# Performance work log

Hardware: AMD Instinct MI355X
Metric: run time of the kernel (lower is better)

Reference implementation:

```python
import jax, jax.numpy as jnp
import numpy as np

N = 50000      # nodes
E = 500000     # edges (avg degree 10)
G = 64         # graphs (events)
IN = 7
H = 64
EPS = 1e-5


def setup_inputs() -> dict:
    key = jax.random.key(0)
    ks = iter(jax.random.split(key, 64))
    d = {}
    d["x"] = jax.random.normal(next(ks), (N, IN), jnp.float32)
    d["edge_index"] = jax.random.randint(next(ks), (2, E), 0, N, dtype=jnp.int32)
    d["batch"] = jnp.sort(jax.random.randint(next(ks), (N,), 0, G, dtype=jnp.int32))
    dims = [(IN, H), (H, 2 * H), (2 * H, 4 * H)]
    for i, (ic, oc) in enumerate(dims, 1):
        d[f"b{i}_W1"] = jax.random.normal(next(ks), (2 * ic, oc), jnp.float32) * 0.05
        d[f"b{i}_b1"] = jnp.zeros((oc,), jnp.float32)
        d[f"b{i}_g1"] = jnp.ones((oc,), jnp.float32)
        d[f"b{i}_beta1"] = jnp.zeros((oc,), jnp.float32)
        d[f"b{i}_W2"] = jax.random.normal(next(ks), (oc, oc), jnp.float32) * 0.05
        d[f"b{i}_b2"] = jnp.zeros((oc,), jnp.float32)
        d[f"b{i}_g2"] = jnp.ones((oc,), jnp.float32)
        d[f"b{i}_beta2"] = jnp.zeros((oc,), jnp.float32)
    d["head_W1"] = jax.random.normal(next(ks), (4 * H, 2 * H), jnp.float32) * 0.05
    d["head_b1"] = jnp.zeros((2 * H,), jnp.float32)
    d["head_W2"] = jax.random.normal(next(ks), (2 * H, 2), jnp.float32) * 0.05
    d["head_b2"] = jnp.zeros((2,), jnp.float32)
    return d


def _bn(h, g, b):
    # BatchNorm1d in training mode: batch statistics over edge dim
    m = h.mean(axis=0)
    v = h.var(axis=0)
    return (h - m) * jax.lax.rsqrt(v + EPS) * g + b


def _edgeconv(x, src, dst, W1, b1, g1, be1, W2, b2, g2, be2):
    # PyG EdgeConv: message = MLP(cat[x_i, x_j - x_i]), aggregated at target i=dst
    xi = x[dst]                                   # [E, C]
    xj = x[src]                                   # [E, C]
    e = jnp.concatenate([xi, xj - xi], axis=-1)   # [E, 2C]
    h = jax.nn.relu(_bn(e @ W1 + b1, g1, be1))
    h = jax.nn.relu(_bn(h @ W2 + b2, g2, be2))
    s = jax.ops.segment_sum(h, dst, num_segments=N)
    cnt = jax.ops.segment_sum(jnp.ones((h.shape[0],), h.dtype), dst, num_segments=N)
    return s / jnp.maximum(cnt, 1.0)[:, None]     # mean aggregation


def reference(x, edge_index, batch,
              b1_W1, b1_b1, b1_g1, b1_beta1, b1_W2, b1_b2, b1_g2, b1_beta2,
              b2_W1, b2_b1, b2_g1, b2_beta1, b2_W2, b2_b2, b2_g2, b2_beta2,
              b3_W1, b3_b1, b3_g1, b3_beta1, b3_W2, b3_b2, b3_g2, b3_beta2,
              head_W1, head_b1, head_W2, head_b2):
    src, dst = edge_index[0], edge_index[1]
    h = _edgeconv(x, src, dst, b1_W1, b1_b1, b1_g1, b1_beta1, b1_W2, b1_b2, b1_g2, b1_beta2)
    h = _edgeconv(h, src, dst, b2_W1, b2_b1, b2_g1, b2_beta1, b2_W2, b2_b2, b2_g2, b2_beta2)
    h = _edgeconv(h, src, dst, b3_W1, b3_b1, b3_g1, b3_beta1, b3_W2, b3_b2, b3_g2, b3_beta2)
    # global mean pool per graph
    s = jax.ops.segment_sum(h, batch, num_segments=G)
    cnt = jax.ops.segment_sum(jnp.ones((N,), h.dtype), batch, num_segments=G)
    g = s / jnp.maximum(cnt, 1.0)[:, None]        # [G, 256]
    # head (dropout is identity in eval)
    z = jax.nn.relu(g @ head_W1 + head_b1)
    return z @ head_W2 + head_b2                  # [G, 2]
```

## Files before the change

kernel.cpp:

```cpp
#include <hip/hip_runtime.h>
#include <stdint.h>

constexpr int NN = 50000;
constexpr int NE = 500000;
constexpr int NG = 64;
constexpr float BN_EPS = 1e-5f;
constexpr int ET = 32;

typedef __attribute__((ext_vector_type(8))) short bf16x8;
typedef __attribute__((ext_vector_type(4))) float f32x4;

__device__ inline float bf2f(unsigned short u) {
    return __uint_as_float(((unsigned int)u) << 16);
}
__device__ inline unsigned short f2bf_rne(float f) {
    unsigned int u = __float_as_uint(f);
    unsigned int r = (u + 0x7fffu + ((u >> 16) & 1u)) >> 16;
    return (unsigned short)r;
}

template<int CPT> __device__ inline void load_row(const float* p, float* o) {
    if constexpr (CPT == 2) { float2 v = *(const float2*)p; o[0]=v.x; o[1]=v.y; }
    else if constexpr (CPT == 4) { float4 v = *(const float4*)p; o[0]=v.x; o[1]=v.y; o[2]=v.z; o[3]=v.w; }
    else { load_row<4>(p, o); load_row<4>(p+4, o+4); }
}
template<int CPT> __device__ inline void store_row(float* p, const float* v) {
    if constexpr (CPT == 2) { *(float2*)p = make_float2(v[0], v[1]); }
    else if constexpr (CPT == 4) { *(float4*)p = make_float4(v[0], v[1], v[2], v[3]); }
    else { store_row<4>(p, v); store_row<4>(p+4, v+4); }
}

__global__ void k_zero16(uint4* p, int n) {
    int i = blockIdx.x * 256 + threadIdx.x;
    if (i < n) p[i] = uint4{0u, 0u, 0u, 0u};
}

__global__ void k_diag(float* out, int n, float val) {
    int i = blockIdx.x * 256 + threadIdx.x;
    if (i < n) out[i] = val;
}

__global__ void k_deg(const int* __restrict__ dst, int* __restrict__ degi) {
    int e = blockIdx.x * 256 + threadIdx.x;
    if (e < NE) atomicAdd(&degi[dst[e]], 1);
}

__global__ void k_scan(const int* __restrict__ degi, int* __restrict__ rowptr) {
    __shared__ int buf[1024];
    __shared__ int carry_s;
    const int tid = threadIdx.x;
    if (tid == 0) carry_s = 0;
    __syncthreads();
    for (int base = 0; base < NN; base += 1024) {
        int i = base + tid;
        int v = (i < NN) ? degi[i] : 0;
        buf[tid] = v;
        __syncthreads();
        for (int off = 1; off < 1024; off <<= 1) {
            int t = (tid >= off) ? buf[tid - off] : 0;
            __syncthreads();
            buf[tid] += t;
            __syncthreads();
        }
        if (i < NN) rowptr[i] = carry_s + buf[tid] - v;
        __syncthreads();
        if (tid == 0) carry_s += buf[1023];
        __syncthreads();
    }
    if (tid == 0) rowptr[NN] = carry_s;
}

__global__ void k_fill(const int* __restrict__ dst, const int* __restrict__ rowptr,
                       int* __restrict__ cursor, int* __restrict__ eidx) {
    int e = blockIdx.x * 256 + threadIdx.x;
    if (e < NE) {
        int d = dst[e];
        int p = atomicAdd(&cursor[d], 1);
        eidx[rowptr[d] + p] = e;
    }
}

__global__ void k_grange(const int* __restrict__ batch, int* __restrict__ gse) {
    int n = blockIdx.x * 256 + threadIdx.x;
    if (n >= NN) return;
    int b = batch[n];
    if (n == 0 || batch[n-1] != b) gse[b] = n;
    if (n == NN-1 || batch[n+1] != b) gse[NG + b] = n + 1;
}

template<int OC>
__global__ void k_bnfin(const float* __restrict__ st, const float* __restrict__ g,
                        const float* __restrict__ be, float* __restrict__ dv) {
    int c = threadIdx.x;
    const float invE = 1.0f / (float)NE;
    float m = st[c] * invE;
    float v = st[OC + c] * invE - m * m;
    float sc = g[c] * rsqrtf(v + BN_EPS);
    dv[c] = sc;
    dv[OC + c] = be[c] - m * sc;
}

template<int OC>
__global__ void k_packW(const float* __restrict__ W,
                        unsigned short* __restrict__ Wph, unsigned short* __restrict__ Wpl) {
    constexpr int NT = OC / 16;
    const int l = threadIdx.x;
    const int ktnt = blockIdx.x;
    const int n = (ktnt % NT) * 16 + (l & 15);
    const int kbase = (ktnt / NT) * 32 + (l >> 4) * 8;
    size_t fo = ((size_t)ktnt * 64 + l) * 8;
    #pragma unroll
    for (int b = 0; b < 8; b++) {
        float w = W[(size_t)(kbase + b) * OC + n];
        unsigned short h = f2bf_rne(w);
        Wph[fo + b] = h;
        Wpl[fo + b] = f2bf_rne(w - bf2f(h));
    }
}

template<int CIN, int OC>
__global__ __launch_bounds__(256) void k_nodeproj(
    const float* __restrict__ x, const float* __restrict__ W1,
    const float* __restrict__ b1, float* __restrict__ A, float* __restrict__ Bn)
{
    constexpr int SP = CIN + 1;
    constexpr int CPT = OC / 32;
    __shared__ float xs[32 * SP];
    const int t = threadIdx.x;
    const int n0 = blockIdx.x * 32;
    {
        const int el = t >> 3, l8 = t & 7;
        int n = n0 + el; if (n >= NN) n = NN - 1;
        const float* xp = x + (size_t)n * CIN;
        for (int k = l8; k < CIN; k += 8) xs[el * SP + k] = xp[k];
    }
    __syncthreads();
    const int tx = t & 31, ty = t >> 5;
    float accA[4][CPT], accB[4][CPT];
    #pragma unroll
    for (int i = 0; i < 4; i++)
        #pragma unroll
        for (int j = 0; j < CPT; j++) { accA[i][j] = 0.f; accB[i][j] = 0.f; }

    const float* Wa = W1 + tx * CPT;
    const float* Wb = W1 + (size_t)CIN * OC + tx * CPT;
    for (int k = 0; k < CIN; k++) {
        float wa[CPT], wb[CPT];
        load_row<CPT>(Wa + (size_t)k * OC, wa);
        load_row<CPT>(Wb + (size_t)k * OC, wb);
        #pragma unroll
        for (int i = 0; i < 4; i++) {
            float ev = xs[(ty * 4 + i) * SP + k];
            #pragma unroll
            for (int j = 0; j < CPT; j++) {
                accA[i][j] = fmaf(ev, wa[j] - wb[j], accA[i][j]);
                accB[i][j] = fmaf(ev, wb[j], accB[i][j]);
            }
        }
    }
    float bs[CPT];
    load_row<CPT>(b1 + tx * CPT, bs);
    #pragma unroll
    for (int i = 0; i < 4; i++) {
        const int n = n0 + ty * 4 + i;
        if (n < NN) {
            float va[CPT];
            #pragma unroll
            for (int j = 0; j < CPT; j++) va[j] = accA[i][j] + bs[j];
            store_row<CPT>(A  + (size_t)n * OC + tx * CPT, va);
            store_row<CPT>(Bn + (size_t)n * OC + tx * CPT, accB[i]);
        }
    }
}

template<int OC>
__global__ __launch_bounds__(256) void k_stats1(
    const float* __restrict__ A, const float* __restrict__ Bn,
    const int* __restrict__ src, const int* __restrict__ dst,
    const int* __restrict__ eidx, float* __restrict__ stats)
{
    constexpr int CPT = OC / 32;
    __shared__ float reds[4 * OC];
    __shared__ float redq[4 * OC];
    const int t = threadIdx.x;
    const int l32 = t & 31, grp = t >> 5;
    float s[CPT], q[CPT];
    #pragma unroll
    for (int j = 0; j < CPT; j++) { s[j] = 0.f; q[j] = 0.f; }
    for (int i = blockIdx.x * 8 + grp; i < NE; i += 8192) {
        const int e = eidx[i];
        float av[CPT], bv[CPT];
        load_row<CPT>(A  + (size_t)dst[e] * OC + l32 * CPT, av);
        load_row<CPT>(Bn + (size_t)src[e] * OC + l32 * CPT, bv);
        #pragma unroll
        for (int j = 0; j < CPT; j++) {
            float h = av[j] + bv[j];
            s[j] += h; q[j] += h * h;
        }
    }
    #pragma unroll
    for (int j = 0; j < CPT; j++) {
        s[j] += __shfl_down(s[j], 32);
        q[j] += __shfl_down(q[j], 32);
    }
    const int w = t >> 6, lane = t & 63;
    if (lane < 32) {
        #pragma unroll
        for (int j = 0; j < CPT; j++) {
            reds[w * OC + lane * CPT + j] = s[j];
            redq[w * OC + lane * CPT + j] = q[j];
        }
    }
    __syncthreads();
    for (int c = t; c < OC; c += 256) {
        float S = reds[c] + reds[OC + c] + reds[2 * OC + c] + reds[3 * OC + c];
        float Q = redq[c] + redq[OC + c] + redq[2 * OC + c] + redq[3 * OC + c];
        atomicAdd(&stats[c], S);
        atomicAdd(&stats[OC + c], Q);
    }
}

template<int OC, int MODE>
__global__ __launch_bounds__(256) void k_efuse(
    const float* __restrict__ A, const float* __restrict__ Bn,
    const int* __restrict__ src, const int* __restrict__ dst,
    const int* __restrict__ eidx,
    const unsigned short* __restrict__ Wph, const unsigned short* __restrict__ Wpl,
    const float* __restrict__ b2,
    const float* __restrict__ dv1, float* __restrict__ stats,
    const float* __restrict__ dv2, float* __restrict__ xout)
{
    constexpr int OCP = OC + 8;
    constexpr int NT = OC / 16, KT = OC / 32, TPW = NT / 2;
    __shared__ __align__(16) unsigned short smem[2 * 32 * OCP];
    __shared__ float sdat[(MODE == 0) ? 2 * OC : 2];
    __shared__ int sdst[ET];
    unsigned short* t_hi = smem;
    unsigned short* t_lo = smem + 32 * OCP;
    float* ytile = (float*)smem;

    const int t = threadIdx.x;
    const int e0 = blockIdx.x * ET;

    if constexpr (MODE == 0) { for (int c = t; c < 2 * OC; c += 256) sdat[c] = 0.f; }

    {
        const int row = t >> 3, l8 = t & 7;
        const int e = eidx[e0 + row];
        const int dn = dst[e], sn = src[e];
        if (l8 == 0) sdst[row] = dn;
        const float* Ar = A  + (size_t)dn * OC;
        const float* Br = Bn + (size_t)sn * OC;
        constexpr int CH = OC / 8;
        const int k0 = l8 * CH;
        #pragma unroll
        for (int k = k0; k < k0 + CH; k += 4) {
            float4 a  = *(const float4*)(Ar + k);
            float4 b  = *(const float4*)(Br + k);
            float4 sc = *(const float4*)(dv1 + k);
            float4 sh = *(const float4*)(dv1 + OC + k);
            float tv[4];
            tv[0] = fmaxf(fmaf(a.x + b.x, sc.x, sh.x), 0.f);
            tv[1] = fmaxf(fmaf(a.y + b.y, sc.y, sh.y), 0.f);
            tv[2] = fmaxf(fmaf(a.z + b.z, sc.z, sh.z), 0.f);
            tv[3] = fmaxf(fmaf(a.w + b.w, sc.w, sh.w), 0.f);
            unsigned short hv[4], lv[4];
            #pragma unroll
            for (int j = 0; j < 4; j++) {
                unsigned short h = f2bf_rne(tv[j]);
                hv[j] = h;
                lv[j] = f2bf_rne(tv[j] - bf2f(h));
            }
            *(ushort4*)(t_hi + row * OCP + k) = *(ushort4*)hv;
            *(ushort4*)(t_lo + row * OCP + k) = *(ushort4*)lv;
        }
    }
    __syncthreads();

    const int wave = t >> 6, lane = t & 63;
    const int rg = wave & 1, half = wave >> 1;
    const int lr = lane & 15, lg = lane >> 4;
    f32x4 acc[TPW];
    #pragma unroll
    for (int j = 0; j < TPW; j++) acc[j] = (f32x4){0.f, 0.f, 0.f, 0.f};
    const unsigned short* ah = t_hi + (rg * 16 + lr) * OCP + lg * 8;
    const unsigned short* al = t_lo + (rg * 16 + lr) * OCP + lg * 8;
    #pragma unroll
    for (int kt = 0; kt < KT; kt++) {
        bf16x8 a_hi = *(const bf16x8*)(ah + kt * 32);
        bf16x8 a_lo = *(const bf16x8*)(al + kt * 32);
        #pragma unroll
        for (int j = 0; j < TPW; j++) {
            const int nt = half * TPW + j;
            const size_t fo = ((size_t)(kt * NT + nt) * 64 + lane) * 8;
            bf16x8 w_hi = *(const bf16x8*)(Wph + fo);
            bf16x8 w_lo = *(const bf16x8*)(Wpl + fo);
            acc[j] = __builtin_amdgcn_mfma_f32_16x16x32_bf16(a_hi, w_hi, acc[j], 0, 0, 0);
            acc[j] = __builtin_amdgcn_mfma_f32_16x16x32_bf16(a_hi, w_lo, acc[j], 0, 0, 0);
            acc[j] = __builtin_amdgcn_mfma_f32_16x16x32_bf16(a_lo, w_hi, acc[j], 0, 0, 0);
        }
    }

    if constexpr (MODE == 0) {
        #pragma unroll
        for (int j = 0; j < TPW; j++) {
            const int col = (half * TPW + j) * 16 + lr;
            const float bb = b2[col];
            float s = 0.f, q = 0.f;
            #pragma unroll
            for (int e = 0; e < 4; e++) { float h = acc[j][e] + bb; s += h; q += h * h; }
            s += __shfl_xor(s, 16); s += __shfl_xor(s, 32);
            q += __shfl_xor(q, 16); q += __shfl_xor(q, 32);
            if (lg == 0) { atomicAdd(&sdat[col], s); atomicAdd(&sdat[OC + col], q); }
        }
        __syncthreads();
        for (int c = t; c < OC; c += 256) {
            atomicAdd(&stats[c], sdat[c]);
            atomicAdd(&stats[OC + c], sdat[OC + c]);
        }
    } else {
        __syncthreads();
        #pragma unroll
        for (int j = 0; j < TPW; j++) {
            const int col = (half * TPW + j) * 16 + lr;
            const float bb = b2[col], sc = dv2[col], sh = dv2[OC + col];
            #pragma unroll
            for (int e = 0; e < 4; e++) {
                const int row = rg * 16 + lg * 4 + e;
                ytile[row * OCP + col] = fmaxf(fmaf(acc[j][e] + bb, sc, sh), 0.f);
            }
        }
        __syncthreads();
        constexpr int STR = 256 / OC;
        constexpr int RS = 32 / STR;
        const int col = t & (OC - 1);
        const int r0 = (t / OC) * RS;
        float a = 0.f; int cur = sdst[r0];
        for (int r = r0; r < r0 + RS; r++) {
            int n = sdst[r];
            if (n != cur) { atomicAdd(&xout[(size_t)cur * OC + col], a); a = 0.f; cur = n; }
            a += ytile[r * OCP + col];
        }
        atomicAdd(&xout[(size_t)cur * OC + col], a);
    }
}

template<int OC>
__global__ __launch_bounds__(256) void k_div(float* __restrict__ xout,
                                             const int* __restrict__ degi) {
    constexpr int CPT = OC / 32;
    const int tx = threadIdx.x & 31;
    const int n = blockIdx.x * 8 + (threadIdx.x >> 5);
    if (n >= NN) return;
    const float inv = 1.0f / fmaxf((float)degi[n], 1.0f);
    float v[CPT];
    load_row<CPT>(xout + (size_t)n * OC + tx * CPT, v);
    #pragma unroll
    for (int j = 0; j < CPT; j++) v[j] *= inv;
    store_row<CPT>(xout + (size_t)n * OC + tx * CPT, v);
}

__global__ void k_pool(const float* __restrict__ x3, const int* __restrict__ gse,
                       float* __restrict__ pooled) {
    const int g = blockIdx.x, c = threadIdx.x;
    const int beg = gse[g], end = gse[NG + g];
    float s = 0.f;
    for (int n = beg; n < end; n++) s += x3[(size_t)n * 256 + c];
    pooled[g * 256 + c] = s / fmaxf((float)(end - beg), 1.0f);
}

__global__ void k_head(const float* __restrict__ pooled,
                       const float* __restrict__ W1, const float* __restrict__ b1,
                       const float* __restrict__ W2, const float* __restrict__ b2,
                       float* __restrict__ out) {
    __shared__ float gv[256];
    __shared__ float z[128];
    const int g = blockIdx.x;
    gv[threadIdx.x] = pooled[g * 256 + threadIdx.x];
    __syncthreads();
    if (threadIdx.x < 128) {
        const int c = threadIdx.x;
        float s = b1[c];
        for (int k = 0; k < 256; k++) s = fmaf(gv[k], W1[k * 128 + c], s);
        z[c] = fmaxf(s, 0.f);
    }
    __syncthreads();
    if (threadIdx.x < 2) {
        const int o = threadIdx.x;
        float s = b2[o];
        for (int k = 0; k < 128; k++) s = fmaf(z[k], W2[k * 2 + o], s);
        out[g * 2 + o] = s;
    }
}

template<int CIN, int OC>
static void run_block(const float* xin, const float* const* Q,
                      float* A, float* B, const int* src, const int* dst,
                      const int* eidx, const unsigned short* Wph, const unsigned short* Wpl,
                      float* st, float* dv, const int* degi,
                      float* xout, hipStream_t s)
{
    k_nodeproj<CIN, OC><<<(NN + 31) / 32, 256, 0, s>>>(xin, Q[0], Q[1], A, B);
    k_stats1<OC><<<1024, 256, 0, s>>>(A, B, src, dst, eidx, st);
    k_bnfin<OC><<<1, OC, 0, s>>>(st, Q[2], Q[3], dv);
    k_efuse<OC, 0><<<NE / ET, 256, 0, s>>>(A, B, src, dst, eidx, Wph, Wpl, Q[5], dv, st + 512, nullptr, nullptr);
    k_bnfin<OC><<<1, OC, 0, s>>>(st + 512, Q[6], Q[7], dv + 512);
    k_zero16<<<((NN * OC / 4) + 255) / 256, 256, 0, s>>>((uint4*)xout, NN * OC / 4);
    k_efuse<OC, 1><<<NE / ET, 256, 0, s>>>(A, B, src, dst, eidx, Wph, Wpl, Q[5], dv, nullptr, dv + 512, xout);
    k_div<OC><<<(NN + 7) / 8, 256, 0, s>>>(xout, degi);
}

extern "C" void kernel_launch(void* const* d_in, const int* in_sizes, int n_in,
                              void* d_out, int out_size, void* d_ws, size_t ws_size,
                              hipStream_t stream)
{
    (void)in_sizes; (void)n_in;
    const float* x = (const float*)d_in[0];
    const int* ei = (const int*)d_in[1];
    const int* src = ei;
    const int* dst = ei + NE;
    const int* batch = (const int*)d_in[2];
    const float* P[28];
    for (int i = 0; i < 28; i++) P[i] = (const float*)d_in[3 + i];
    float* out = (float*)d_out;

    size_t offs[18];
    {
        size_t o = 0;
        auto take = [&](size_t bytes) -> size_t {
            size_t r = o; o = (o + bytes + 255) & ~(size_t)255; return r;
        };
        offs[0] = take((size_t)NN * 256 * 4);
        offs[1] = take((size_t)NN * 256 * 4);
        offs[2] = take((size_t)NN * 256 * 4);
        offs[3] = take((size_t)NN * 128 * 4);
        offs[4] = o;
        offs[5] = take((size_t)NN * 4);
        offs[6] = take((size_t)NN * 4);
        offs[7] = take(3 * 1024 * 4);
        offs[8] = take(2 * NG * 4);
        offs[9] = o;
        offs[10] = take((size_t)(NN + 1) * 4);
        offs[11] = take((size_t)NE * 4);
        offs[12] = take(3 * 1024 * 4);
        offs[13] = take((size_t)NG * 256 * 4);
        offs[14] = take((64*64 + 128*128 + 256*256) * 2);
        offs[15] = take((64*64 + 128*128 + 256*256) * 2);
        offs[16] = o;
        if (ws_size < o) {
            float val = 1000.0f + (float)(ws_size >> 20);
            k_diag<<<(out_size + 255) / 256, 256, 0, stream>>>(out, out_size, val);
            return;
        }
    }

    char* W = (char*)d_ws;
    float* A  = (float*)(W + offs[0]);
    float* B  = (float*)(W + offs[1]);
    float* xa = (float*)(W + offs[2]);
    float* xb = (float*)(W + offs[3]);
    int* degi = (int*)(W + offs[5]);
    int* cursor = (int*)(W + offs[6]);
    float* stats = (float*)(W + offs[7]);
    int* gse = (int*)(W + offs[8]);
    int* rowptr = (int*)(W + offs[10]);
    int* eidx = (int*)(W + offs[11]);
    float* dv = (float*)(W + offs[12]);
    float* pooled = (float*)(W + offs[13]);
    unsigned short* Wph = (unsigned short*)(W + offs[14]);
    unsigned short* Wpl = (unsigned short*)(W + offs[15]);
    unsigned short* Wph1 = Wph,            * Wpl1 = Wpl;
    unsigned short* Wph2 = Wph + 64*64,    * Wpl2 = Wpl + 64*64;
    unsigned short* Wph3 = Wph2 + 128*128, * Wpl3 = Wpl2 + 128*128;

    int nz = (int)((offs[9] - offs[4]) / 16);
    k_zero16<<<(nz + 255) / 256, 256, 0, stream>>>((uint4*)(W + offs[4]), nz);

    k_deg<<<(NE + 255) / 256, 256, 0, stream>>>(dst, degi);
    k_scan<<<1, 1024, 0, stream>>>(degi, rowptr);
    k_fill<<<(NE + 255) / 256, 256, 0, stream>>>(dst, rowptr, cursor, eidx);
    k_grange<<<(NN + 255) / 256, 256, 0, stream>>>(batch, gse);

    k_packW<64> <<<(64/32)*(64/16),   64, 0, stream>>>(P[4],  Wph1, Wpl1);
    k_packW<128><<<(128/32)*(128/16), 64, 0, stream>>>(P[12], Wph2, Wpl2);
    k_packW<256><<<(256/32)*(256/16), 64, 0, stream>>>(P[20], Wph3, Wpl3);

    run_block<7,   64>(x,  P + 0,  A, B, src, dst, eidx, Wph1, Wpl1, stats + 0,    dv + 0,    degi, xa, stream);
    run_block<64, 128>(xa, P + 8,  A, B, src, dst, eidx, Wph2, Wpl2, stats + 1024, dv + 1024, degi, xb, stream);
    run_block<128,256>(xb, P + 16, A, B, src, dst, eidx, Wph3, Wpl3, stats + 2048, dv + 2048, degi, xa, stream);

    k_pool<<<NG, 256, 0, stream>>>(xa, gse, pooled);
    k_head<<<NG, 256, 0, stream>>>(pooled, P[24], P[25], P[26], P[27], out);
}
```

Measured before the change: 3.024 ms.

## Retile edge MLP kernel to 128 edges per block with K-chunked swizzled LDS

The fused edge kernel now handles 128 edges per block instead of 32. Each wave computes a 4x(NT/2) grid of MFMA tiles, so every weight fragment loaded from global memory is reused across four row tiles. The A operand is staged in 64-column K chunks in an XOR-swizzled LDS buffer to avoid bank conflicts, and the mean-aggregation scatter runs in row strips. This cuts weight reloads and block count, at the cost of more registers per thread (launch bounds target 2 blocks), more barriers, and removal of the shared-memory pre-reduction of BN stats, which now go straight to global atomics.

```diff
diff --git a/kernel.cpp b/kernel.cpp
--- a/kernel.cpp
+++ b/kernel.cpp
@@ -5,7 +5,6 @@
 constexpr int NE = 500000;
 constexpr int NG = 64;
 constexpr float BN_EPS = 1e-5f;
-constexpr int ET = 32;
 
 typedef __attribute__((ext_vector_type(8))) short bf16x8;
 typedef __attribute__((ext_vector_type(4))) float f32x4;
@@ -221,7 +220,7 @@
 }
 
 template<int OC, int MODE>
-__global__ __launch_bounds__(256) void k_efuse(
+__global__ __launch_bounds__(256, 2) void k_efuse(
     const float* __restrict__ A, const float* __restrict__ Bn,
     const int* __restrict__ src, const int* __restrict__ dst,
     const int* __restrict__ eidx,
@@ -230,118 +229,173 @@
     const float* __restrict__ dv1, float* __restrict__ stats,
     const float* __restrict__ dv2, float* __restrict__ xout)
 {
-    constexpr int OCP = OC + 8;
-    constexpr int NT = OC / 16, KT = OC / 32, TPW = NT / 2;
-    __shared__ __align__(16) unsigned short smem[2 * 32 * OCP];
-    __shared__ float sdat[(MODE == 0) ? 2 * OC : 2];
-    __shared__ int sdst[ET];
-    unsigned short* t_hi = smem;
-    unsigned short* t_lo = smem + 32 * OCP;
-    float* ytile = (float*)smem;
+    constexpr int ETL = 128;
+    constexpr int NT = OC / 16;
+    constexpr int NTW = NT / 2;
+    constexpr int NCH = OC / 64;
+    constexpr int SROWS = 8192 / OC;
+    constexpr int NSTRIP = ETL / SROWS;
+    constexpr int YSTR = OC + 4;
+    constexpr int YB = SROWS * YSTR * 4;
+    constexpr int SMB = (MODE == 1 && YB > 32768) ? YB : 32768;
+
+    __shared__ __align__(16) unsigned char smem[SMB];
+    __shared__ int sdst_s[ETL], ssrc_s[ETL];
 
     const int t = threadIdx.x;
-    const int e0 = blockIdx.x * ET;
-
-    if constexpr (MODE == 0) { for (int c = t; c < 2 * OC; c += 256) sdat[c] = 0.f; }
-
-    {
-        const int row = t >> 3, l8 = t & 7;
-        const int e = eidx[e0 + row];
-        const int dn = dst[e], sn = src[e];
-        if (l8 == 0) sdst[row] = dn;
-        const float* Ar = A  + (size_t)dn * OC;
-        const float* Br = Bn + (size_t)sn * OC;
-        constexpr int CH = OC / 8;
-        const int k0 = l8 * CH;
-        #pragma unroll
-        for (int k = k0; k < k0 + CH; k += 4) {
-            float4 a  = *(const float4*)(Ar + k);
-            float4 b  = *(const float4*)(Br + k);
-            float4 sc = *(const float4*)(dv1 + k);
-            float4 sh = *(const float4*)(dv1 + OC + k);
-            float tv[4];
-            tv[0] = fmaxf(fmaf(a.x + b.x, sc.x, sh.x), 0.f);
-            tv[1] = fmaxf(fmaf(a.y + b.y, sc.y, sh.y), 0.f);
-            tv[2] = fmaxf(fmaf(a.z + b.z, sc.z, sh.z), 0.f);
-            tv[3] = fmaxf(fmaf(a.w + b.w, sc.w, sh.w), 0.f);
-            unsigned short hv[4], lv[4];
+    const int e0 = blockIdx.x * ETL;
+    const int valid = (NE - e0 < ETL) ? (NE - e0) : ETL;
+
+    if (t < ETL) {
+        int dn = -1, sn = -1;
+        if (t < valid) { int e = eidx[e0 + t]; dn = dst[e]; sn = src[e]; }
+        sdst_s[t] = dn; ssrc_s[t] = sn;
+    }
+    __syncthreads();
+
+    const int lane = t & 63, wave = t >> 6;
+    const int rg = wave >> 1, ch = wave & 1;
+    const int lr = lane & 15, lg = lane >> 4;
+
+    f32x4 acc[4][NTW];
+    #pragma unroll
+    for (int m = 0; m < 4; m++)
+        #pragma unroll
+        for (int n = 0; n < NTW; n++) acc[m][n] = (f32x4){0.f, 0.f, 0.f, 0.f};
+
+    const int brow = t >> 1, bhf = t & 1;
+
+    for (int kc = 0; kc < NCH; kc++) {
+        {
+            const int gc0 = kc * 64 + bhf * 32;
+            if (brow < valid) {
+                const float* Ar  = A  + (size_t)sdst_s[brow] * OC + gc0;
+                const float* Br  = Bn + (size_t)ssrc_s[brow] * OC + gc0;
+                const float* scp = dv1 + gc0;
+                const float* shp = dv1 + OC + gc0;
+                #pragma unroll
+                for (int i = 0; i < 8; i++) {
+                    float4 a  = *(const float4*)(Ar + i * 4);
+                    float4 b  = *(const float4*)(Br + i * 4);
+                    float4 sc = *(const float4*)(scp + i * 4);
+                    float4 sh = *(const float4*)(shp + i * 4);
+                    float tv[4];
+                    tv[0] = fmaxf(fmaf(a.x + b.x, sc.x, sh.x), 0.f);
+                    tv[1] = fmaxf(fmaf(a.y + b.y, sc.y, sh.y), 0.f);
+                    tv[2] = fmaxf(fmaf(a.z + b.z, sc.z, sh.z), 0.f);
+                    tv[3] = fmaxf(fmaf(a.w + b.w, sc.w, sh.w), 0.f);
+                    unsigned short hv[4], lv[4];
+                    #pragma unroll
+                    for (int j = 0; j < 4; j++) {
+                        unsigned short h = f2bf_rne(tv[j]);
+                        hv[j] = h;
+                        lv[j] = f2bf_rne(tv[j] - bf2f(h));
+                    }
+                    const int byt = (brow * 128 + bhf * 64 + i * 8) ^ ((brow & 7) << 4);
+                    *(ushort4*)(smem + byt) = *(ushort4*)hv;
+                    *(ushort4*)(smem + 16384 + byt) = *(ushort4*)lv;
+                }
+            } else {
+                const ushort4 z = ushort4{0, 0, 0, 0};
+                #pragma unroll
+                for (int i = 0; i < 8; i++) {
+                    const int byt = (brow * 128 + bhf * 64 + i * 8) ^ ((brow & 7) << 4);
+                    *(ushort4*)(smem + byt) = z;
+                    *(ushort4*)(smem + 16384 + byt) = z;
+                }
+            }
+        }
+        __syncthreads();
+
+        #pragma unroll
+        for (int kt2 = 0; kt2 < 2; kt2++) {
+            bf16x8 ah[4], al[4];
             #pragma unroll
-            for (int j = 0; j < 4; j++) {
-                unsigned short h = f2bf_rne(tv[j]);
-                hv[j] = h;
-                lv[j] = f2bf_rne(tv[j] - bf2f(h));
-            }
-            *(ushort4*)(t_hi + row * OCP + k) = *(ushort4*)hv;
-            *(ushort4*)(t_lo + row * OCP + k) = *(ushort4*)lv;
-        }
-    }
-    __syncthreads();
-
-    const int wave = t >> 6, lane = t & 63;
-    const int rg = wave & 1, half = wave >> 1;
-    const int lr = lane & 15, lg = lane >> 4;
-    f32x4 acc[TPW];
-    #pragma unroll
-    for (int j = 0; j < TPW; j++) acc[j] = (f32x4){0.f, 0.f, 0.f, 0.f};
-    const unsigned short* ah = t_hi + (rg * 16 + lr) * OCP + lg * 8;
-    const unsigned short* al = t_lo + (rg * 16 + lr) * OCP + lg * 8;
-    #pragma unroll
-    for (int kt = 0; kt < KT; kt++) {
-        bf16x8 a_hi = *(const bf16x8*)(ah + kt * 32);
-        bf16x8 a_lo = *(const bf16x8*)(al + kt * 32);
-        #pragma unroll
-        for (int j = 0; j < TPW; j++) {
-            const int nt = half * TPW + j;
-            const size_t fo = ((size_t)(kt * NT + nt) * 64 + lane) * 8;
-            bf16x8 w_hi = *(const bf16x8*)(Wph + fo);
-            bf16x8 w_lo = *(const bf16x8*)(Wpl + fo);
-            acc[j] = __builtin_amdgcn_mfma_f32_16x16x32_bf16(a_hi, w_hi, acc[j], 0, 0, 0);
-            acc[j] = __builtin_amdgcn_mfma_f32_16x16x32_bf16(a_hi, w_lo, acc[j], 0, 0, 0);
-            acc[j] = __builtin_amdgcn_mfma_f32_16x16x32_bf16(a_lo, w_hi, acc[j], 0, 0, 0);
-        }
+            for (int m = 0; m < 4; m++) {
+                const int r = rg * 64 + m * 16 + lr;
+                const int byt = (r * 128 + kt2 * 64 + lg * 16) ^ ((r & 7) << 4);
+                ah[m] = *(const bf16x8*)(smem + byt);
+                al[m] = *(const bf16x8*)(smem + 16384 + byt);
+            }
+            #pragma unroll
+            for (int n = 0; n < NTW; n++) {
+                const size_t fo = ((size_t)((kc * 2 + kt2) * NT + ch * NTW + n) * 64 + lane) * 8;
+                bf16x8 wh = *(const bf16x8*)(Wph + fo);
+                bf16x8 wl = *(const bf16x8*)(Wpl + fo);
+                #pragma unroll
+                for (int m = 0; m < 4; m++) {
+                    acc[m][n] = __builtin_amdgcn_mfma_f32_16x16x32_bf16(ah[m], wh, acc[m][n], 0, 0, 0);
+                    acc[m][n] = __builtin_amdgcn_mfma_f32_16x16x32_bf16(ah[m], wl, acc[m][n], 0, 0, 0);
+                    acc[m][n] = __builtin_amdgcn_mfma_f32_16x16x32_bf16(al[m], wh, acc[m][n], 0, 0, 0);
+                }
+            }
+        }
+        __syncthreads();
     }
 
     if constexpr (MODE == 0) {
         #pragma unroll
-        for (int j = 0; j < TPW; j++) {
-            const int col = (half * TPW + j) * 16 + lr;
+        for (int n = 0; n < NTW; n++) {
+            const int col = ch * (OC / 2) + n * 16 + lr;
             const float bb = b2[col];
             float s = 0.f, q = 0.f;
             #pragma unroll
-            for (int e = 0; e < 4; e++) { float h = acc[j][e] + bb; s += h; q += h * h; }
+            for (int m = 0; m < 4; m++) {
+                const int rbase = rg * 64 + m * 16 + lg * 4;
+                #pragma unroll
+                for (int e = 0; e < 4; e++) {
+                    float h = (rbase + e < valid) ? (acc[m][n][e] + bb) : 0.f;
+                    s += h; q += h * h;
+                }
+            }
             s += __shfl_xor(s, 16); s += __shfl_xor(s, 32);
             q += __shfl_xor(q, 16); q += __shfl_xor(q, 32);
-            if (lg == 0) { atomicAdd(&sdat[col], s); atomicAdd(&sdat[OC + col], q); }
-        }
-        __syncthreads();
-        for (int c = t; c < OC; c += 256) {
-            atomicAdd(&stats[c], sdat[c]);
-            atomicAdd(&stats[OC + c], sdat[OC + c]);
+            if (lg == 0) {
+                atomicAdd(&stats[col], s);
+                atomicAdd(&stats[OC + col], q);
+            }
         }
     } else {
-        __syncthreads();
-        #pragma unroll
-        for (int j = 0; j < TPW; j++) {
-            const int col = (half * TPW + j) * 16 + lr;
-            const float bb = b2[col], sc = dv2[col], sh = dv2[OC + col];
+        float* yt = (float*)smem;
+        const int acol = t % OC;
+        const int aseg = t / OC;
+        #pragma unroll
+        for (int s = 0; s < NSTRIP; s++) {
+            const int r0 = s * SROWS;
             #pragma unroll
-            for (int e = 0; e < 4; e++) {
-                const int row = rg * 16 + lg * 4 + e;
-                ytile[row * OCP + col] = fmaxf(fmaf(acc[j][e] + bb, sc, sh), 0.f);
-            }
-        }
-        __syncthreads();
-        constexpr int STR = 256 / OC;
-        constexpr int RS = 32 / STR;
-        const int col = t & (OC - 1);
-        const int r0 = (t / OC) * RS;
-        float a = 0.f; int cur = sdst[r0];
-        for (int r = r0; r < r0 + RS; r++) {
-            int n = sdst[r];
-            if (n != cur) { atomicAdd(&xout[(size_t)cur * OC + col], a); a = 0.f; cur = n; }
-            a += ytile[r * OCP + col];
-        }
-        atomicAdd(&xout[(size_t)cur * OC + col], a);
+            for (int m = 0; m < 4; m++) {
+                const int base = rg * 64 + m * 16;
+                if (base >= r0 && base < r0 + SROWS) {
+                    #pragma unroll
+                    for (int n = 0; n < NTW; n++) {
+                        const int col = ch * (OC / 2) + n * 16 + lr;
+                        const float bb = b2[col], scv = dv2[col], shv = dv2[OC + col];
+                        #pragma unroll
+                        for (int e = 0; e < 4; e++) {
+                            const int rl = base - r0 + lg * 4 + e;
+                            yt[rl * YSTR + col] = fmaxf(fmaf(acc[m][n][e] + bb, scv, shv), 0.f);
+                        }
+                    }
+                }
+            }
+            __syncthreads();
+            {
+                const int rbeg = aseg * 32;
+                float a = 0.f; int cur = -1;
+                for (int r = 0; r < 32; r++) {
+                    const int gr = r0 + rbeg + r;
+                    if (gr >= valid) break;
+                    const int nd = sdst_s[gr];
+                    if (nd != cur) {
+                        if (cur >= 0) atomicAdd(&xout[(size_t)cur * OC + acol], a);
+                        cur = nd; a = 0.f;
+                    }
+                    a += yt[(rbeg + r) * YSTR + acol];
+                }
+                if (cur >= 0) atomicAdd(&xout[(size_t)cur * OC + acol], a);
+            }
+            __syncthreads();
+        }
     }
 }
 
@@ -400,13 +454,14 @@
                       float* st, float* dv, const int* degi,
                       float* xout, hipStream_t s)
 {
+    const int EG = (NE + 127) / 128;
     k_nodeproj<CIN, OC><<<(NN + 31) / 32, 256, 0, s>>>(xin, Q[0], Q[1], A, B);
     k_stats1<OC><<<1024, 256, 0, s>>>(A, B, src, dst, eidx, st);
     k_bnfin<OC><<<1, OC, 0, s>>>(st, Q[2], Q[3], dv);
-    k_efuse<OC, 0><<<NE / ET, 256, 0, s>>>(A, B, src, dst, eidx, Wph, Wpl, Q[5], dv, st + 512, nullptr, nullptr);
+    k_efuse<OC, 0><<<EG, 256, 0, s>>>(A, B, src, dst, eidx, Wph, Wpl, Q[5], dv, st + 512, nullptr, nullptr);
     k_bnfin<OC><<<1, OC, 0, s>>>(st + 512, Q[6], Q[7], dv + 512);
     k_zero16<<<((NN * OC / 4) + 255) / 256, 256, 0, s>>>((uint4*)xout, NN * OC / 4);
-    k_efuse<OC, 1><<<NE / ET, 256, 0, s>>>(A, B, src, dst, eidx, Wph, Wpl, Q[5], dv, nullptr, dv + 512, xout);
+    k_efuse<OC, 1><<<EG, 256, 0, s>>>(A, B, src, dst, eidx, Wph, Wpl, Q[5], dv, nullptr, dv + 512, xout);
     k_div<OC><<<(NN + 7) / 8, 256, 0, s>>>(xout, degi);
 }
 
```

Result: faster. 2.704 ms (-10.6%).
